# Kernel tuning notes

Hardware: AMD Instinct MI355X
Metric: run time of the kernel (lower is better)

## Reference

```python
import jax, jax.numpy as jnp
import numpy as np

HEAD_NUM = 4
EMB = 128
N_NODES = 50000
N_EDGES = 600000


def setup_inputs() -> dict:
    key = jax.random.key(0)
    k1, k2, k3, k4, k5, k6 = jax.random.split(key, 6)
    embeds = jax.random.normal(k1, (N_NODES, EMB), dtype=jnp.float32)
    qW = jax.random.normal(k2, (EMB, EMB), dtype=jnp.float32) * (1.0 / np.sqrt(EMB))
    kW = jax.random.normal(k3, (EMB, EMB), dtype=jnp.float32) * (1.0 / np.sqrt(EMB))
    vW = jax.random.normal(k4, (EMB, EMB), dtype=jnp.float32) * (1.0 / np.sqrt(EMB))
    rows = jax.random.randint(k5, (N_EDGES,), 0, N_NODES, dtype=jnp.int32)
    cols = jax.random.randint(k6, (N_EDGES,), 0, N_NODES, dtype=jnp.int32)
    return {"embeds": embeds, "qW": qW, "kW": kW, "vW": vW,
            "rows": rows, "cols": cols, "n_nodes": N_NODES}


def reference(embeds, qW, kW, vW, rows, cols, n_nodes):
    H = HEAD_NUM
    D = embeds.shape[1]
    Dh = D // H
    rowEmb = embeds[rows]                                   # [E, D] gather
    colEmb = embeds[cols]                                   # [E, D] gather
    q = (rowEmb @ qW).reshape(-1, H, Dh)                    # [E, H, Dh]
    k = (colEmb @ kW).reshape(-1, H, Dh)
    v = (colEmb @ vW).reshape(-1, H, Dh)
    att = jnp.einsum('ehd,ehd->eh', q, k)                   # per-edge per-head logits
    att = jnp.clip(att, -10.0, 10.0)
    expAtt = jnp.exp(att)                                   # [E, H]
    attNorm = jax.ops.segment_sum(expAtt, rows, num_segments=n_nodes)  # [N, H]
    att = expAtt / (attNorm[rows] + 1e-8)                   # segment softmax
    res = (att[..., None] * v).reshape(-1, D)               # [E, D]
    out = jax.ops.segment_sum(res, rows, num_segments=n_nodes)  # [N, D]
    return out
```

## Files before the change

kernel.cpp:

```cpp
#include <hip/hip_runtime.h>
#include <math.h>

#define EMB 128
#define HEADS 4
#define ROWSTRIDE 152
#define OSTRIDE 260
#define CAP 64

typedef __attribute__((ext_vector_type(8))) _Float16 f16x8;
typedef __attribute__((ext_vector_type(4))) _Float16 f16x4;
typedef __attribute__((ext_vector_type(4))) float f32x4;

__global__ __launch_bounds__(256) void prep_w(
    const float* __restrict__ Wq, const float* __restrict__ Wk, const float* __restrict__ Wv,
    _Float16* __restrict__ Wfrag)
{
    int flat = blockIdx.x * 256 + threadIdx.x;
    int m    = flat >> 14;
    int rem  = flat & 16383;
    int ct   = rem >> 11;
    int s    = (rem >> 9) & 3;
    int lane = (rem >> 3) & 63;
    int j    = rem & 7;
    int k = s * 32 + (lane >> 4) * 8 + j;
    int n = ct * 16 + (lane & 15);
    const float* Ws[3] = { Wq, Wk, Wv };
    Wfrag[flat] = (_Float16)Ws[m][k * 128 + n];
}

__global__ __launch_bounds__(256) void mega_kernel(
    const float* __restrict__ embeds,
    const _Float16* __restrict__ Wfrag,
    _Float16* __restrict__ Qh, _Float16* __restrict__ KV,
    const int* __restrict__ rows, const int* __restrict__ cols,
    int* __restrict__ deg, unsigned short* __restrict__ slots,
    int N, int E, int PB, int S)
{
    __shared__ __align__(16) _Float16 sBuf[64 * OSTRIDE];

    const int bid = blockIdx.x;
    const bool isProj = ((bid % S) == 0) && ((bid / S) < PB);

    if (!isProj) {
        int fidx = bid - min((bid + S - 1) / S, PB);
        int e = fidx * 256 + threadIdx.x;
        if (e < E) {
            int r = rows[e];
            int pos = atomicAdd(&deg[r], 1);
            if (pos < CAP) slots[(size_t)r * CAP + pos] = (unsigned short)cols[e];
        }
        return;
    }

    const int n0 = (bid / S) * 64;
    const int t  = threadIdx.x;

    #pragma unroll
    for (int j = 0; j < 8; j++) {
        int flat = t + j * 256;
        int row  = flat >> 5;
        int c4   = flat & 31;
        int gn   = n0 + row;
        float4 v = (gn < N) ? reinterpret_cast<const float4*>(embeds)[(size_t)gn * 32 + c4]
                            : make_float4(0.f, 0.f, 0.f, 0.f);
        f16x4 u = { (_Float16)v.x, (_Float16)v.y, (_Float16)v.z, (_Float16)v.w };
        *reinterpret_cast<f16x4*>(&sBuf[row * ROWSTRIDE + c4 * 4]) = u;
    }
    __syncthreads();

    const int w    = t >> 6;
    const int lane = t & 63;
    const int nlo  = lane & 15;
    const int quad = lane >> 4;

    f16x8 a[4];
    #pragma unroll
    for (int s = 0; s < 4; s++) {
        int row = 16 * w + nlo;
        int k   = s * 32 + quad * 8;
        a[s] = *reinterpret_cast<const f16x8*>(&sBuf[row * ROWSTRIDE + k]);
    }
    __syncthreads();

    const int rowL = 16 * w + quad * 4;

    #pragma unroll
    for (int ct = 0; ct < 8; ct++) {
        f32x4 acc = { 0.f, 0.f, 0.f, 0.f };
        #pragma unroll
        for (int s = 0; s < 4; s++) {
            f16x8 b = *reinterpret_cast<const f16x8*>(
                Wfrag + ((size_t)(ct * 4 + s) * 64 + lane) * 8);
            acc = __builtin_amdgcn_mfma_f32_16x16x32_f16(a[s], b, acc, 0, 0, 0);
        }
        int col = ct * 16 + nlo;
        #pragma unroll
        for (int r = 0; r < 4; r++)
            sBuf[(rowL + r) * OSTRIDE + col] = (_Float16)acc[r];
    }
    __syncthreads();
    #pragma unroll
    for (int j = 0; j < 4; j++) {
        int flat = j * 2048 + t * 8;
        int row  = flat >> 7;
        int col  = flat & 127;
        int gn   = n0 + row;
        if (gn < N) {
            f16x8 v = *reinterpret_cast<const f16x8*>(&sBuf[row * OSTRIDE + col]);
            *reinterpret_cast<f16x8*>(&Qh[(size_t)gn * EMB + col]) = v;
        }
    }
    __syncthreads();

    #pragma unroll
    for (int m = 1; m < 3; m++) {
        int voff = (m == 2) ? 4 : 0;
        #pragma unroll
        for (int ct = 0; ct < 8; ct++) {
            f32x4 acc = { 0.f, 0.f, 0.f, 0.f };
            #pragma unroll
            for (int s = 0; s < 4; s++) {
                f16x8 b = *reinterpret_cast<const f16x8*>(
                    Wfrag + ((size_t)((m * 8 + ct) * 4 + s) * 64 + lane) * 8);
                acc = __builtin_amdgcn_mfma_f32_16x16x32_f16(a[s], b, acc, 0, 0, 0);
            }
            int col  = ct * 16 + nlo;
            int lidx = 8 * (col >> 2) + (col & 3) + voff;
            #pragma unroll
            for (int r = 0; r < 4; r++)
                sBuf[(rowL + r) * OSTRIDE + lidx] = (_Float16)acc[r];
        }
    }
    __syncthreads();
    #pragma unroll
    for (int j = 0; j < 8; j++) {
        int flat = j * 2048 + t * 8;
        int row  = flat >> 8;
        int col  = flat & 255;
        int gn   = n0 + row;
        if (gn < N) {
            f16x8 v = *reinterpret_cast<const f16x8*>(&sBuf[row * OSTRIDE + col]);
            *reinterpret_cast<f16x8*>(&KV[(size_t)gn * 256 + col]) = v;
        }
    }
}

__global__ __launch_bounds__(256) void node_fused(
    const _Float16* __restrict__ Qh, const _Float16* __restrict__ KV,
    const int* __restrict__ deg, const unsigned short* __restrict__ slots,
    float* __restrict__ out, int N)
{
    int n = blockIdx.x * 8 + (threadIdx.x >> 5);
    if (n >= N) return;
    int lane = threadIdx.x & 31;

    f16x4 qh = *reinterpret_cast<const f16x4*>(Qh + (size_t)n * EMB + lane * 4);
    float qx = (float)qh.x, qy = (float)qh.y, qz = (float)qh.z, qw = (float)qh.w;

    int cnt = deg[n];
    if (cnt > CAP) cnt = CAP;
    const unsigned short* sl = slots + (size_t)n * CAP;

    float4 acc = make_float4(0.f, 0.f, 0.f, 0.f);
    float norm = 0.f;

    const _Float16* KVl = KV + 8 * lane;
    int i = 0;

    for (; i + 4 <= cnt; i += 4) {
        int c0 = sl[i], c1 = sl[i + 1], c2 = sl[i + 2], c3 = sl[i + 3];
        f16x8 kv0 = *reinterpret_cast<const f16x8*>(KVl + (size_t)c0 * 256);
        f16x8 kv1 = *reinterpret_cast<const f16x8*>(KVl + (size_t)c1 * 256);
        f16x8 kv2 = *reinterpret_cast<const f16x8*>(KVl + (size_t)c2 * 256);
        f16x8 kv3 = *reinterpret_cast<const f16x8*>(KVl + (size_t)c3 * 256);

        float d0 = qx * (float)kv0[0] + qy * (float)kv0[1] + qz * (float)kv0[2] + qw * (float)kv0[3];
        float d1 = qx * (float)kv1[0] + qy * (float)kv1[1] + qz * (float)kv1[2] + qw * (float)kv1[3];
        float d2 = qx * (float)kv2[0] + qy * (float)kv2[1] + qz * (float)kv2[2] + qw * (float)kv2[3];
        float d3 = qx * (float)kv3[0] + qy * (float)kv3[1] + qz * (float)kv3[2] + qw * (float)kv3[3];
        d0 += __shfl_xor(d0, 1); d1 += __shfl_xor(d1, 1); d2 += __shfl_xor(d2, 1); d3 += __shfl_xor(d3, 1);
        d0 += __shfl_xor(d0, 2); d1 += __shfl_xor(d1, 2); d2 += __shfl_xor(d2, 2); d3 += __shfl_xor(d3, 2);
        d0 += __shfl_xor(d0, 4); d1 += __shfl_xor(d1, 4); d2 += __shfl_xor(d2, 4); d3 += __shfl_xor(d3, 4);

        float ea0 = exp2f(fminf(10.f, fmaxf(-10.f, d0)) * 1.44269504f);
        float ea1 = exp2f(fminf(10.f, fmaxf(-10.f, d1)) * 1.44269504f);
        float ea2 = exp2f(fminf(10.f, fmaxf(-10.f, d2)) * 1.44269504f);
        float ea3 = exp2f(fminf(10.f, fmaxf(-10.f, d3)) * 1.44269504f);

        acc.x = fmaf(ea0, (float)kv0[4], acc.x);
        acc.y = fmaf(ea0, (float)kv0[5], acc.y);
        acc.z = fmaf(ea0, (float)kv0[6], acc.z);
        acc.w = fmaf(ea0, (float)kv0[7], acc.w);
        acc.x = fmaf(ea1, (float)kv1[4], acc.x);
        acc.y = fmaf(ea1, (float)kv1[5], acc.y);
        acc.z = fmaf(ea1, (float)kv1[6], acc.z);
        acc.w = fmaf(ea1, (float)kv1[7], acc.w);
        acc.x = fmaf(ea2, (float)kv2[4], acc.x);
        acc.y = fmaf(ea2, (float)kv2[5], acc.y);
        acc.z = fmaf(ea2, (float)kv2[6], acc.z);
        acc.w = fmaf(ea2, (float)kv2[7], acc.w);
        acc.x = fmaf(ea3, (float)kv3[4], acc.x);
        acc.y = fmaf(ea3, (float)kv3[5], acc.y);
        acc.z = fmaf(ea3, (float)kv3[6], acc.z);
        acc.w = fmaf(ea3, (float)kv3[7], acc.w);
        norm += ea0 + ea1 + ea2 + ea3;
    }
    for (; i < cnt; i++) {
        int c0 = sl[i];
        f16x8 kv0 = *reinterpret_cast<const f16x8*>(KVl + (size_t)c0 * 256);
        float d0 = qx * (float)kv0[0] + qy * (float)kv0[1] + qz * (float)kv0[2] + qw * (float)kv0[3];
        d0 += __shfl_xor(d0, 1);
        d0 += __shfl_xor(d0, 2);
        d0 += __shfl_xor(d0, 4);
        float ea0 = exp2f(fminf(10.f, fmaxf(-10.f, d0)) * 1.44269504f);
        acc.x = fmaf(ea0, (float)kv0[4], acc.x);
        acc.y = fmaf(ea0, (float)kv0[5], acc.y);
        acc.z = fmaf(ea0, (float)kv0[6], acc.z);
        acc.w = fmaf(ea0, (float)kv0[7], acc.w);
        norm += ea0;
    }

    float inv = 1.f / (norm + 1e-8f);
    acc.x *= inv; acc.y *= inv; acc.z *= inv; acc.w *= inv;
    reinterpret_cast<float4*>(out + (size_t)n * EMB)[lane] = acc;
}

extern "C" void kernel_launch(void* const* d_in, const int* in_sizes, int n_in,
                              void* d_out, int out_size, void* d_ws, size_t ws_size,
                              hipStream_t stream) {
    const float* embeds = (const float*)d_in[0];
    const float* qW     = (const float*)d_in[1];
    const float* kW     = (const float*)d_in[2];
    const float* vW     = (const float*)d_in[3];
    const int*   rows   = (const int*)d_in[4];
    const int*   cols   = (const int*)d_in[5];

    const int N = in_sizes[0] / EMB;
    const int E = in_sizes[4];

    _Float16*       Qh    = (_Float16*)d_ws;
    _Float16*       KV    = Qh + (size_t)N * EMB;
    _Float16*       Wfrag = KV + (size_t)N * 256;
    int*            deg   = (int*)(Wfrag + 3 * 16384);
    unsigned short* slots = (unsigned short*)(deg + N);

    float* out = (float*)d_out;

    (void)hipMemsetAsync(deg, 0, (size_t)N * sizeof(int), stream);

    prep_w<<<192, 256, 0, stream>>>(qW, kW, vW, Wfrag);

    const int PB = (N + 63) / 64;
    const int FB = (E + 255) / 256;
    const int S  = (PB + FB) / PB > 1 ? (PB + FB) / PB : 1;
    mega_kernel<<<PB + FB, 256, 0, stream>>>(embeds, Wfrag, Qh, KV,
                                             rows, cols, deg, slots, N, E, PB, S);

    node_fused<<<(N + 7) / 8, 256, 0, stream>>>(Qh, KV, deg, slots, out, N);
}
```

Measured before the change: 172.0 us.

## Restructure projection so each wave loads weight fragments once across all row strips

Each wave used to load A fragments for its own 16-row strip and then stream every weight fragment for Q, K and V. Now each wave holds A fragments for all four strips in registers and owns six of the 24 column tiles, so every weight fragment is read from global memory once per block instead of four times. Q, K and V are all staged in one larger shared buffer before write-out, which removes two barriers. In exchange, register pressure rises (16 A vectors plus 4 B vectors per thread) and shared memory grows from about 33KB to about 50KB per block, which may lower occupancy for the projection blocks.

```diff
diff --git a/kernel.cpp b/kernel.cpp
--- a/kernel.cpp
+++ b/kernel.cpp
@@ -4,7 +4,7 @@
 #define EMB 128
 #define HEADS 4
 #define ROWSTRIDE 152
-#define OSTRIDE 260
+#define OSTRIDE2 388
 #define CAP 64
 
 typedef __attribute__((ext_vector_type(8))) _Float16 f16x8;
@@ -36,7 +36,7 @@
     int* __restrict__ deg, unsigned short* __restrict__ slots,
     int N, int E, int PB, int S)
 {
-    __shared__ __align__(16) _Float16 sBuf[64 * OSTRIDE];
+    __shared__ __align__(16) _Float16 sBuf[64 * OSTRIDE2];
 
     const int bid = blockIdx.x;
     const bool isProj = ((bid % S) == 0) && ((bid / S) < PB);
@@ -73,32 +73,47 @@
     const int nlo  = lane & 15;
     const int quad = lane >> 4;
 
-    f16x8 a[4];
-    #pragma unroll
-    for (int s = 0; s < 4; s++) {
-        int row = 16 * w + nlo;
-        int k   = s * 32 + quad * 8;
-        a[s] = *reinterpret_cast<const f16x8*>(&sBuf[row * ROWSTRIDE + k]);
-    }
+    f16x8 a[4][4];
+    #pragma unroll
+    for (int strip = 0; strip < 4; strip++)
+        #pragma unroll
+        for (int s = 0; s < 4; s++)
+            a[strip][s] = *reinterpret_cast<const f16x8*>(
+                &sBuf[(16 * strip + nlo) * ROWSTRIDE + s * 32 + quad * 8]);
     __syncthreads();
 
-    const int rowL = 16 * w + quad * 4;
-
-    #pragma unroll
-    for (int ct = 0; ct < 8; ct++) {
-        f32x4 acc = { 0.f, 0.f, 0.f, 0.f };
+    const int rbase = quad * 4;
+
+    #pragma unroll
+    for (int u = 0; u < 6; u++) {
+        const int T  = w + u * 4;
+        const int m  = T >> 3;
+        const int ct = T & 7;
+
+        f16x8 b[4];
         #pragma unroll
-        for (int s = 0; s < 4; s++) {
-            f16x8 b = *reinterpret_cast<const f16x8*>(
-                Wfrag + ((size_t)(ct * 4 + s) * 64 + lane) * 8);
-            acc = __builtin_amdgcn_mfma_f32_16x16x32_f16(a[s], b, acc, 0, 0, 0);
-        }
-        int col = ct * 16 + nlo;
+        for (int s = 0; s < 4; s++)
+            b[s] = *reinterpret_cast<const f16x8*>(
+                Wfrag + ((size_t)(T * 4 + s) * 64 + lane) * 8);
+
+        const int col  = ct * 16 + nlo;
+        const int lcol = (m == 0) ? col
+                                  : 128 + 8 * (col >> 2) + (col & 3) + ((m == 2) ? 4 : 0);
+
         #pragma unroll
-        for (int r = 0; r < 4; r++)
-            sBuf[(rowL + r) * OSTRIDE + col] = (_Float16)acc[r];
+        for (int strip = 0; strip < 4; strip++) {
+            f32x4 acc = { 0.f, 0.f, 0.f, 0.f };
+            #pragma unroll
+            for (int s = 0; s < 4; s++)
+                acc = __builtin_amdgcn_mfma_f32_16x16x32_f16(a[strip][s], b[s], acc, 0, 0, 0);
+            const int row = 16 * strip + rbase;
+            #pragma unroll
+            for (int r = 0; r < 4; r++)
+                sBuf[(row + r) * OSTRIDE2 + lcol] = (_Float16)acc[r];
+        }
     }
     __syncthreads();
+
     #pragma unroll
     for (int j = 0; j < 4; j++) {
         int flat = j * 2048 + t * 8;
@@ -106,32 +121,10 @@
         int col  = flat & 127;
         int gn   = n0 + row;
         if (gn < N) {
-            f16x8 v = *reinterpret_cast<const f16x8*>(&sBuf[row * OSTRIDE + col]);
+            f16x8 v = *reinterpret_cast<const f16x8*>(&sBuf[row * OSTRIDE2 + col]);
             *reinterpret_cast<f16x8*>(&Qh[(size_t)gn * EMB + col]) = v;
         }
     }
-    __syncthreads();
-
-    #pragma unroll
-    for (int m = 1; m < 3; m++) {
-        int voff = (m == 2) ? 4 : 0;
-        #pragma unroll
-        for (int ct = 0; ct < 8; ct++) {
-            f32x4 acc = { 0.f, 0.f, 0.f, 0.f };
-            #pragma unroll
-            for (int s = 0; s < 4; s++) {
-                f16x8 b = *reinterpret_cast<const f16x8*>(
-                    Wfrag + ((size_t)((m * 8 + ct) * 4 + s) * 64 + lane) * 8);
-                acc = __builtin_amdgcn_mfma_f32_16x16x32_f16(a[s], b, acc, 0, 0, 0);
-            }
-            int col  = ct * 16 + nlo;
-            int lidx = 8 * (col >> 2) + (col & 3) + voff;
-            #pragma unroll
-            for (int r = 0; r < 4; r++)
-                sBuf[(rowL + r) * OSTRIDE + lidx] = (_Float16)acc[r];
-        }
-    }
-    __syncthreads();
     #pragma unroll
     for (int j = 0; j < 8; j++) {
         int flat = j * 2048 + t * 8;
@@ -139,7 +132,7 @@
         int col  = flat & 255;
         int gn   = n0 + row;
         if (gn < N) {
-            f16x8 v = *reinterpret_cast<const f16x8*>(&sBuf[row * OSTRIDE + col]);
+            f16x8 v = *reinterpret_cast<const f16x8*>(&sBuf[row * OSTRIDE2 + 128 + col]);
             *reinterpret_cast<f16x8*>(&KV[(size_t)gn * 256 + col]) = v;
         }
     }
```

New measurement: 174.4 us. About the same (+1.4%).
